# Kernel optimization log

Hardware: AMD Instinct MI355X
Metric: run time of the kernel (lower is better)

The kernel has to match this reference:

```python
import jax, jax.numpy as jnp
import numpy as np

B, N, S, NS, V = 4, 4096, 1024, 32, 8
CIN, COUT = 64, 128
RADIUS = 0.2
C1 = CIN + 6  # cin + grouped_xyz(3) + local_xyz(3)
EPS = 1e-5


def _bn(x, g, b):
    # training-mode batchnorm over all axes except the trailing channel axis
    axes = tuple(range(x.ndim - 1))
    m = jnp.mean(x, axes, keepdims=True)
    v = jnp.var(x, axes, keepdims=True)
    return (x - m) * jax.lax.rsqrt(v + EPS) * g + b


def _fps(xyz, s):
    # farthest point sampling, deterministic start at index 0
    b, n, _ = xyz.shape
    bar = jnp.arange(b)
    def step(carry, _):
        mind, last = carry
        p = xyz[bar, last]  # [B,3]
        d = jnp.sum((xyz - p[:, None, :]) ** 2, -1)
        mind = jnp.minimum(mind, d)
        nxt = jnp.argmax(mind, -1).astype(jnp.int32)
        return (mind, nxt), nxt
    idx0 = jnp.zeros((b,), jnp.int32)
    _, rest = jax.lax.scan(step, (jnp.full((b, n), 1e10, xyz.dtype), idx0), None, length=s - 1)
    idx = jnp.concatenate([idx0[None], rest], 0).T  # [B,S]
    return jnp.take_along_axis(xyz, idx[..., None], axis=1), idx


def _ball_query(new_xyz, xyz, k, radius):
    # first-k-in-index-order points within radius; -1 padding like pytorch3d
    n = xyz.shape[1]
    d2 = jnp.sum((new_xyz[:, :, None, :] - xyz[:, None, :, :]) ** 2, -1)  # [B,S,N]
    key = jnp.where(d2 < radius * radius, jnp.arange(n, dtype=jnp.int32), n)
    negk, _ = jax.lax.top_k(-key, k)  # k smallest keys
    idx = -negk
    mask = idx >= n
    return jnp.where(mask, -1, idx), mask


def _masked_gather(x, idx):
    # gather rows of x [B,N,C] at idx [B,S,k]; zeros where idx == -1
    b, s, k = idx.shape
    safe = jnp.maximum(idx, 0).reshape(b, s * k)
    g = jnp.take_along_axis(x, safe[..., None], axis=1).reshape(b, s, k, x.shape[-1])
    return jnp.where((idx == -1)[..., None], 0.0, g)


def setup_inputs() -> dict:
    key = jax.random.key(0)
    ks = jax.random.split(key, 10)
    xyz = jax.random.uniform(ks[0], (B, N, 3), jnp.float32)
    f = jax.random.normal(ks[1], (B, N, CIN), jnp.float32)
    # cube-corner frame points, scaled by radius*0.8, rotated about Y (as in __init__)
    corners = jnp.array([[x, y, z] for x in (-1.0, 1.0) for y in (-1.0, 1.0) for z in (-1.0, 1.0)], jnp.float32)
    ang = jax.random.uniform(ks[2], ()) * 2.0 * jnp.pi
    c, sn = jnp.cos(ang), jnp.sin(ang)
    z, o = jnp.zeros(()), jnp.ones(())
    rot = jnp.stack([jnp.stack([c, z, sn]), jnp.stack([z, o, z]), jnp.stack([-sn, z, c])])
    framepoints = (corners * (RADIUS * 0.8)) @ rot.T
    w = lambda k_, sh: jax.random.normal(k_, sh, jnp.float32) * 0.05
    return {
        "xyz": xyz, "f": f, "framepoints": framepoints,
        "w1_0": w(ks[3], (13, 64)), "b1_0": jnp.zeros((64,), jnp.float32),
        "g1_0": jnp.ones((64,), jnp.float32), "bt1_0": jnp.zeros((64,), jnp.float32),
        "w1_1": w(ks[4], (64, C1)), "b1_1": jnp.zeros((C1,), jnp.float32),
        "w2_0": w(ks[5], (C1, 128)), "b2_0": jnp.zeros((128,), jnp.float32),
        "g2_0": jnp.ones((128,), jnp.float32), "bt2_0": jnp.zeros((128,), jnp.float32),
        "w2_1": w(ks[6], (128, COUT)), "b2_1": jnp.zeros((COUT,), jnp.float32),
        "res_w": w(ks[7], (CIN, COUT)), "res_b": jnp.zeros((COUT,), jnp.float32),
    }


def _forward(xyz, f, framepoints, w1_0, b1_0, g1_0, bt1_0, w1_1, b1_1,
             w2_0, b2_0, g2_0, bt2_0, w2_1, b2_1, res_w, res_b):
    new_xyz, _ = _fps(xyz, S)                           # [B,S,3]
    idx, mask = _ball_query(new_xyz, xyz, NS, RADIUS)   # [B,S,NS]
    grouped_xyz = _masked_gather(xyz, idx)              # [B,S,NS,3]
    grouped_feature = _masked_gather(f, idx)            # [B,S,NS,CIN]
    local = grouped_xyz - new_xyz[:, :, None, :]
    gf = jnp.concatenate([grouped_xyz, local, grouped_feature], -1)   # [B,S,NS,C1]
    arrow = grouped_xyz[:, :, :, None, :] - framepoints               # [B,S,NS,V,3]
    euc = jnp.sqrt(jnp.sum(arrow ** 2, -1, keepdims=True))
    gx = jnp.broadcast_to(grouped_xyz[:, :, :, None, :], arrow.shape)
    fp = jnp.broadcast_to(framepoints, arrow.shape)
    coc = jnp.concatenate([-arrow, arrow, euc, gx, fp], -1)           # [B,S,NS,V,13]
    # m1: per-point MLP (1x1x1 Conv3d) 13 -> 64 (bn+relu) -> C1
    a = jax.nn.relu(_bn(coc @ w1_0 + b1_0, g1_0, bt1_0))
    a = a @ w1_1 + b1_1                                               # [B,S,NS,V,C1]
    # frame-modulated features + softmax attention over the V frame axis
    p = gf[:, :, :, None, :] * a                                      # [B,S,NS,V,C1]
    agg = jnp.sum(jax.nn.softmax(p, axis=3) * p, axis=3)              # [B,S,NS,C1]
    agg = jnp.where(mask[..., None], 0.0, agg)
    # m2: per-point MLP (1x1 Conv2d) C1 -> 128 (bn+relu) -> COUT
    wmid = jax.nn.relu(_bn(agg @ w2_0 + b2_0, g2_0, bt2_0))
    wout = wmid @ w2_1 + b2_1                                         # [B,S,NS,COUT]
    new_f = jax.nn.gelu(wout + grouped_feature @ res_w + res_b, approximate=False)
    return jnp.max(new_f, axis=2), new_xyz


def reference(xyz, f, framepoints, w1_0, b1_0, g1_0, bt1_0, w1_1, b1_1,
              w2_0, b2_0, g2_0, bt2_0, w2_1, b2_1, res_w, res_b):
    return _forward(xyz, f, framepoints, w1_0, b1_0, g1_0, bt1_0, w1_1, b1_1,
                    w2_0, b2_0, g2_0, bt2_0, w2_1, b2_1, res_w, res_b)
```

## Files before the change

kernel.cpp:

```cpp
#include <hip/hip_runtime.h>
#include <hip/hip_bf16.h>
#include <math.h>

typedef __hip_bfloat16 bf16;
typedef __attribute__((ext_vector_type(8))) short short8;
typedef __attribute__((ext_vector_type(4))) float f32x4;
typedef unsigned long long u64;

#define BB  4
#define NN  4096
#define SS  1024
#define KNS 32
#define C1  70

__device__ __forceinline__ float b2f(bf16 x){ return __bfloat162float(x); }

__device__ __forceinline__ float ld(const void* p, size_t i, bool F){
    return F ? ((const float*)p)[i] : __bfloat162float(((const bf16*)p)[i]);
}
__device__ __forceinline__ void st(void* p, size_t i, float v, bool F){
    if (F) ((float*)p)[i] = v; else ((bf16*)p)[i] = __float2bfloat16(v);
}
__device__ __forceinline__ unsigned short f2us(float x){
    __hip_bfloat16 h = __float2bfloat16(x);
    return *reinterpret_cast<unsigned short*>(&h);
}
__device__ __forceinline__ float us2f(unsigned short u){
    return __uint_as_float(((unsigned)u) << 16);
}
__device__ __forceinline__ float fast_gelu(float x){
    float xs = x * 0.70710678118654752f;
    float ax = fabsf(xs);
    float t = 1.0f / fmaf(0.3275911f, ax, 1.0f);
    float poly = fmaf(fmaf(fmaf(fmaf(1.061405429f, t, -1.453152027f), t,
                    1.421413741f), t, -0.284496736f), t, 0.254829592f) * t;
    float er = 1.0f - poly * __expf(-ax*ax);
    er = copysignf(er, xs);
    return 0.5f * x * (1.0f + er);
}

__device__ __forceinline__ u64 pk_add(u64 a, u64 b){
    u64 d;
    asm("v_pk_add_f32 %0, %1, %2" : "=v"(d) : "v"(a), "v"(b));
    return d;
}
__device__ __forceinline__ u64 pk_mul(u64 a, u64 b){
    u64 d;
    asm("v_pk_mul_f32 %0, %1, %2" : "=v"(d) : "v"(a), "v"(b));
    return d;
}
__device__ __forceinline__ u64 pack2f(float a, float b){
    return (((u64)__float_as_uint(b)) << 32) | __float_as_uint(a);
}
__device__ __forceinline__ u64 dup2f(float a){
    unsigned u = __float_as_uint(a);
    return (((u64)u) << 32) | u;
}

#define DPP_STEP(key, CTRL) do{ \
    int _a = __builtin_amdgcn_update_dpp(0, (int)(unsigned)(key), CTRL, 0xF, 0xF, true); \
    int _b = __builtin_amdgcn_update_dpp(0, (int)(unsigned)((key) >> 32), CTRL, 0xF, 0xF, true); \
    u64 _o = (((u64)(unsigned)_b) << 32) | (unsigned)_a; \
    if (_o > (key)) (key) = _o; }while(0)
#define SWZ_STEP(key, OFF) do{ \
    int _a = __builtin_amdgcn_ds_swizzle((int)(unsigned)(key), OFF); \
    int _b = __builtin_amdgcn_ds_swizzle((int)(unsigned)((key) >> 32), OFF); \
    u64 _o = (((u64)(unsigned)_b) << 32) | (unsigned)_a; \
    if (_o > (key)) (key) = _o; }while(0)

__global__ __launch_bounds__(256) void fps_kernel(const void* __restrict__ xyz,
        float* __restrict__ nxf, void* __restrict__ out, int* __restrict__ flag){
    __shared__ float4 pts[NN];
    __shared__ int sidx[SS];
    __shared__ u64 skey[2][4];
    __shared__ int scnt;
    const int b = blockIdx.x, t = threadIdx.x, lane = t & 63, w = t >> 6;
    if (t == 0) scnt = 0;
    __syncthreads();
    {
        int c = 0;
        for (int i = t; i < 2048; i += 256){
            float v = __bfloat162float(((const bf16*)xyz)[i]);
            if (!(fabsf(v) <= 1.5f)) c++;
        }
        atomicAdd(&scnt, c);
    }
    __syncthreads();
    const bool F = (scnt > 10);
    if (b == 0 && t == 0) *flag = F ? 1 : 0;

    u64 px2[8], py2[8], pz2[8];
    float mind[16];
#pragma unroll
    for (int j = 0; j < 8; j++){
        int i0 = (2*j)*256 + t, i1 = (2*j+1)*256 + t;
        float X0 = ld(xyz, (size_t)(b*NN+i0)*3+0, F);
        float Y0 = ld(xyz, (size_t)(b*NN+i0)*3+1, F);
        float Z0 = ld(xyz, (size_t)(b*NN+i0)*3+2, F);
        float X1 = ld(xyz, (size_t)(b*NN+i1)*3+0, F);
        float Y1 = ld(xyz, (size_t)(b*NN+i1)*3+1, F);
        float Z1 = ld(xyz, (size_t)(b*NN+i1)*3+2, F);
        pts[i0] = make_float4(X0, Y0, Z0, 0.f);
        pts[i1] = make_float4(X1, Y1, Z1, 0.f);
        px2[j] = pack2f(X0, X1); py2[j] = pack2f(Y0, Y1); pz2[j] = pack2f(Z0, Z1);
        mind[2*j] = 1e10f; mind[2*j+1] = 1e10f;
    }
    if (t == 0) sidx[0] = 0;
    __syncthreads();
    float4 q = pts[0];
    for (int s = 1; s < SS; s++){
        const u64 nx2 = dup2f(-q.x), ny2 = dup2f(-q.y), nz2 = dup2f(-q.z);
        float bd = -1.f; int bi = 0;
#pragma unroll
        for (int j = 0; j < 8; j++){
            u64 dx2 = pk_add(px2[j], nx2);
            u64 dy2 = pk_add(py2[j], ny2);
            u64 dz2 = pk_add(pz2[j], nz2);
            u64 d2 = pk_add(pk_add(pk_mul(dx2,dx2), pk_mul(dy2,dy2)), pk_mul(dz2,dz2));
            float dlo = __uint_as_float((unsigned)d2);
            float dhi = __uint_as_float((unsigned)(d2 >> 32));
            float m0 = fminf(mind[2*j], dlo); mind[2*j] = m0;
            if (m0 > bd){ bd = m0; bi = (2*j)*256 + t; }
            float m1 = fminf(mind[2*j+1], dhi); mind[2*j+1] = m1;
            if (m1 > bd){ bd = m1; bi = (2*j+1)*256 + t; }
        }
        u64 key = ((u64)__float_as_uint(bd) << 32) | (unsigned)(~bi);
        DPP_STEP(key, 0xB1);
        DPP_STEP(key, 0x4E);
        DPP_STEP(key, 0x128);
        SWZ_STEP(key, 0x101F);
        SWZ_STEP(key, 0x401F);
        {
            u64 o = __shfl_xor(key, 32);
            if (o > key) key = o;
        }
        const int par = s & 1;
        if (lane == 0) skey[par][w] = key;
        __syncthreads();
        u64 k0 = skey[par][0], k1 = skey[par][1];
        u64 k2 = skey[par][2], k3 = skey[par][3];
        if (k1 > k0) k0 = k1;
        if (k3 > k2) k2 = k3;
        if (k2 > k0) k0 = k2;
        int ix = (int)(~(unsigned)(k0 & 0xffffffffull));
        if (t == 0) sidx[s] = ix;
        q = pts[ix];
    }
    __syncthreads();
    const size_t o1 = (size_t)BB*SS*128;
    for (int s2 = t; s2 < SS; s2 += 256){
        int i = sidx[s2];
        float4 p = pts[i];
        nxf[(b*SS+s2)*3+0] = p.x; nxf[(b*SS+s2)*3+1] = p.y; nxf[(b*SS+s2)*3+2] = p.z;
        st(out, o1 + (size_t)(b*SS+s2)*3+0, p.x, F);
        st(out, o1 + (size_t)(b*SS+s2)*3+1, p.y, F);
        st(out, o1 + (size_t)(b*SS+s2)*3+2, p.z, F);
    }
}

__global__ __launch_bounds__(512) void ball_kernel(const void* __restrict__ xyz,
        const float* __restrict__ nxf, int* __restrict__ idx, const int* __restrict__ flag){
    __shared__ float sx[NN], sy[NN], sz[NN];
    const bool F = (*flag != 0);
    const int b = blockIdx.x, t = threadIdx.x, lane = t & 63, w = t >> 6;
    for (int i = t; i < NN; i += 512){
        sx[i] = ld(xyz, (size_t)(b*NN+i)*3+0, F);
        sy[i] = ld(xyz, (size_t)(b*NN+i)*3+1, F);
        sz[i] = ld(xyz, (size_t)(b*NN+i)*3+2, F);
    }
    __syncthreads();
    const float R2 = 0.2f*0.2f;
    const u64 below = (lane == 63) ? ~0ull >> 1 : ((1ull << lane) - 1ull);
#pragma unroll
    for (int cc = 0; cc < 4; cc++){
        const int s = blockIdx.y*32 + w*4 + cc;
        const float px = nxf[(b*SS+s)*3+0];
        const float py = nxf[(b*SS+s)*3+1];
        const float pz = nxf[(b*SS+s)*3+2];
        int* op = idx + (size_t)(b*SS+s)*KNS;
        int cnt = 0;
        for (int c = 0; c < 64; c++){
            const int i = c*64 + lane;
            float dx = __fsub_rn(px, sx[i]);
            float dy = __fsub_rn(py, sy[i]);
            float dz = __fsub_rn(pz, sz[i]);
            float d2 = __fadd_rn(__fadd_rn(__fmul_rn(dx,dx), __fmul_rn(dy,dy)), __fmul_rn(dz,dz));
            const bool hit = (d2 < R2);
            u64 m = __ballot(hit);
            if (hit){
                int pos = cnt + __popcll(m & below);
                if (pos < KNS) op[pos] = i;
            }
            cnt += __popcll(m);
            if (cnt >= KNS) break;
        }
        if (lane < KNS && lane >= cnt) op[lane] = -1;
    }
}

__device__ __forceinline__ void pack_frag(int e, int K, const void* W, bool F,
                                          short* H, short* L){
    int j = e & 7, lane = (e >> 3) & 63, nt = (e >> 9) & 7, kt = e >> 12;
    int k = kt*32 + ((lane >> 4) & 3)*8 + j;
    int n = nt*16 + (lane & 15);
    float v = (k < K) ? ld(W, (size_t)k*128 + n, F) : 0.f;
    unsigned short h = f2us(v);
    unsigned short l2 = f2us(v - us2f(h));
    H[e] = (short)h; L[e] = (short)l2;
}

__global__ __launch_bounds__(256) void prep1_kernel(
        const void* __restrict__ w20, const void* __restrict__ w21,
        const void* __restrict__ rw, const void* __restrict__ b20,
        const void* __restrict__ b21, const void* __restrict__ rb,
        short* __restrict__ w20rp_h, short* __restrict__ w20rp_l,
        short* __restrict__ w21p_h, short* __restrict__ w21p_l,
        short* __restrict__ rwp_h, short* __restrict__ rwp_l,
        float* __restrict__ b20r, float* __restrict__ bof,
        double* __restrict__ M, double* __restrict__ sums, const int* __restrict__ flag){
    const bool F = (*flag != 0);
    const int t = threadIdx.x;
    if (blockIdx.x == 0){
        if (t < 105) M[t] = 0.0;
        if (t < 256) sums[t] = 0.0;
    }
    int e = blockIdx.x*256 + t;
    if (e < 12288){ pack_frag(e, 70, w20, F, w20rp_h, w20rp_l); return; }
    e -= 12288;
    if (e < 16384){ pack_frag(e, 128, w21, F, w21p_h, w21p_l); return; }
    e -= 16384;
    if (e < 8192){ pack_frag(e, 64, rw, F, rwp_h, rwp_l); return; }
    e -= 8192;
    if (e < 128){
        b20r[e] = ld(b20, e, F);
        bof[e]  = ld(b21, e, F) + ld(rb, e, F);
    }
}

__global__ __launch_bounds__(256) void bn1_stats(const void* __restrict__ xyz,
        const int* __restrict__ idx, const void* __restrict__ fpt, double* __restrict__ M,
        const int* __restrict__ flag){
    __shared__ float sfp[24];
    const bool F = (*flag != 0);
    const int t = threadIdx.x, lane = t & 63;
    if (t < 24) sfp[t] = ld(fpt, t, F);
    __syncthreads();
    float acc[66];
#pragma unroll
    for (int q = 0; q < 66; q++) acc[q] = 0.f;
    for (int it = 0; it < 4; it++){
        const int row = blockIdx.x*1024 + it*256 + t;
        const int b = row >> 15;
        const int id = idx[row];
        float gx = 0.f, gy = 0.f, gz = 0.f;
        if (id >= 0){
            gx = ld(xyz, (size_t)(b*NN+id)*3+0, F);
            gy = ld(xyz, (size_t)(b*NN+id)*3+1, F);
            gz = ld(xyz, (size_t)(b*NN+id)*3+2, F);
        }
#pragma unroll
        for (int v = 0; v < 8; v++){
            float fxv = sfp[v*3+0], fyv = sfp[v*3+1], fzv = sfp[v*3+2];
            float ax = gx - fxv, ay = gy - fyv, az = gz - fzv;
            float eu = sqrtf(ax*ax + ay*ay + az*az);
            float f11[11];
            f11[0] = ax; f11[1] = ay; f11[2] = az; f11[3] = eu;
            f11[4] = gx; f11[5] = gy; f11[6] = gz;
            f11[7] = fxv; f11[8] = fyv; f11[9] = fzv; f11[10] = 1.0f;
            int q = 0;
#pragma unroll
            for (int i = 0; i < 11; i++)
#pragma unroll
                for (int j = i; j < 11; j++){
                    acc[q] = fmaf(f11[i], f11[j], acc[q]);
                    q++;
                }
        }
    }
#pragma unroll
    for (int q = 0; q < 66; q++){
        float s = acc[q];
#pragma unroll
        for (int off = 1; off < 64; off <<= 1) s += __shfl_xor(s, off);
        if (lane == 0) atomicAdd(&M[q], (double)s);
    }
}

__global__ __launch_bounds__(256) void m1_kernel(
        const void* __restrict__ xyz, const void* __restrict__ f, const void* __restrict__ fpt,
        const void* __restrict__ w10, const void* __restrict__ b10,
        const void* __restrict__ w11, const void* __restrict__ b11,
        const float* __restrict__ nxf, const int* __restrict__ idx,
        const double* __restrict__ M, const void* __restrict__ g1, const void* __restrict__ bt1,
        float* __restrict__ agg, const int* __restrict__ flag){
    __shared__ short sthi[4*2*8*72];
    __shared__ short stlo[4*2*8*72];
    __shared__ float gfb[4*2*80];
    __shared__ double Ms[11][11];
    __shared__ float bn1s[128];
    __shared__ short Bh_l[2*5*64*8];
    __shared__ short Bl_l[2*5*64*8];
    const bool F = (*flag != 0);
    const int t = threadIdx.x, lane = t & 63, w = t >> 6;
    const int kq = lane >> 4, cn = lane & 15;

    if (t < 66){
        int e = t, i = 0, off = 0;
        while (e - off >= 11 - i){ off += 11 - i; i++; }
        int j = i + (e - off);
        double val = M[t];
        Ms[i][j] = val; Ms[j][i] = val;
    }
    for (int e = t; e < 2*5*64*8; e += 256){
        int j = e & 7, le = (e >> 3) & 63, rest = e >> 9;
        int nt = rest % 5, ks = rest / 5;
        int k = ks*32 + (le >> 4)*8 + j;
        int c = nt*16 + (le & 15);
        float wv = (c < C1) ? ld(w11, (size_t)k*C1 + c, F) : 0.f;
        unsigned short h = f2us(wv);
        unsigned short l2 = f2us(wv - us2f(h));
        Bh_l[e] = (short)h; Bl_l[e] = (short)l2;
    }
    __syncthreads();
    if (t < 64){
        const double K = 1048576.0;
        const int    bi14[14] = {0,1,2, 0,1,2, 3, 4,5,6, 7,8,9, 10};
        const double sg14[14] = {-1,-1,-1, 1,1,1, 1, 1,1,1, 1,1,1, 1};
        double mv14[14];
        for (int i = 0; i < 14; i++) mv14[i] = sg14[i] * Ms[bi14[i]][10] / K;
        double wc[13];
        for (int i = 0; i < 13; i++) wc[i] = (double)ld(w10, i*64+t, F);
        double mean = (double)ld(b10, t, F);
        for (int i = 0; i < 13; i++) mean += mv14[i]*wc[i];
        double var = 0.0;
        for (int i = 0; i < 13; i++)
            for (int j = 0; j < 13; j++){
                double mij = sg14[i]*sg14[j]*Ms[bi14[i]][bi14[j]]/K;
                var += wc[i]*wc[j]*(mij - mv14[i]*mv14[j]);
            }
        float sc = ld(g1, t, F) / sqrtf((float)var + 1e-5f);
        bn1s[t] = sc;
        bn1s[64+t] = ld(bt1, t, F) - (float)mean * sc;
    }
    __syncthreads();
    const float sc1 = bn1s[lane], sh1 = bn1s[64+lane];

    float binit[5];
#pragma unroll
    for (int nt = 0; nt < 5; nt++){
        int c = nt*16 + cn;
        binit[nt] = (c < C1) ? ld(b11, c, F) : 0.f;
    }
    float W10c[13];
#pragma unroll
    for (int i = 0; i < 13; i++) W10c[i] = ld(w10, i*64+lane, F);
    const float b10v = ld(b10, lane, F);
    float fx[8], fy[8], fz[8];
#pragma unroll
    for (int v = 0; v < 8; v++){
        fx[v] = ld(fpt, v*3+0, F); fy[v] = ld(fpt, v*3+1, F); fz[v] = ld(fpt, v*3+2, F);
    }
    const int quad = lane >> 4;
    const int rr = quad >> 1;
    const int hh = quad & 1;
    const int mA = lane & 15;
    const int rA = mA >> 3, vA = mA & 7;

    const int wid = blockIdx.x*4 + w;
    for (int p = 0; p < 16; p++){
        const int rowbase = wid*32 + p*2;
        int ids[2];
#pragma unroll
        for (int r = 0; r < 2; r++){
            const int row = rowbase + r;
            const int b = row >> 15, s = (row >> 5) & 1023;
            const int id = idx[row];
            ids[r] = id;
            float gx = 0.f, gy = 0.f, gz = 0.f, fv0 = 0.f, fv1 = 0.f;
            if (id >= 0){
                gx = ld(xyz, (size_t)(b*NN+id)*3+0, F);
                gy = ld(xyz, (size_t)(b*NN+id)*3+1, F);
                gz = ld(xyz, (size_t)(b*NN+id)*3+2, F);
                if (lane >= 6) fv0 = ld(f, (size_t)(b*NN+id)*64 + (lane-6), F);
                if (lane < 6)  fv1 = ld(f, (size_t)(b*NN+id)*64 + (58+lane), F);
            }
            const float nxx = nxf[(b*SS+s)*3+0], nxy = nxf[(b*SS+s)*3+1], nxz = nxf[(b*SS+s)*3+2];
            float gf0;
            if (lane == 0) gf0 = gx; else if (lane == 1) gf0 = gy; else if (lane == 2) gf0 = gz;
            else if (lane == 3) gf0 = gx - nxx; else if (lane == 4) gf0 = gy - nxy;
            else if (lane == 5) gf0 = gz - nxz; else gf0 = fv0;
            gfb[w*160 + r*80 + lane] = gf0;
            if (lane < 6)       gfb[w*160 + r*80 + 64 + lane] = fv1;
            else if (lane < 16) gfb[w*160 + r*80 + 64 + lane] = 0.f;
            const int sb = ((w*2 + r)*8)*72 + lane;
#pragma unroll
            for (int v = 0; v < 8; v++){
                float ax = gx - fx[v], ay = gy - fy[v], az = gz - fz[v];
                float eu = sqrtf(ax*ax + ay*ay + az*az);
                float z = b10v;
                z = fmaf(-ax, W10c[0], z); z = fmaf(-ay, W10c[1], z); z = fmaf(-az, W10c[2], z);
                z = fmaf( ax, W10c[3], z); z = fmaf( ay, W10c[4], z); z = fmaf( az, W10c[5], z);
                z = fmaf( eu, W10c[6], z);
                z = fmaf( gx, W10c[7], z); z = fmaf( gy, W10c[8], z); z = fmaf( gz, W10c[9], z);
                z = fmaf(fx[v], W10c[10], z); z = fmaf(fy[v], W10c[11], z); z = fmaf(fz[v], W10c[12], z);
                float a1 = fmaxf(fmaf(z, sc1, sh1), 0.f);
                unsigned short h = f2us(a1);
                unsigned short l2 = f2us(a1 - us2f(h));
                sthi[sb + v*72] = (short)h;
                stlo[sb + v*72] = (short)l2;
            }
        }
        f32x4 acc[5];
#pragma unroll
        for (int nt = 0; nt < 5; nt++){
            f32x4 a; a[0] = binit[nt]; a[1] = binit[nt]; a[2] = binit[nt]; a[3] = binit[nt];
            acc[nt] = a;
        }
        const int aoff = ((w*2 + rA)*8 + vA)*72 + kq*8;
#pragma unroll
        for (int ks = 0; ks < 2; ks++){
            short8 ahi = *(const short8*)&sthi[aoff + ks*32];
            short8 alo = *(const short8*)&stlo[aoff + ks*32];
#pragma unroll
            for (int nt = 0; nt < 5; nt++){
                short8 Wh = ((const short8*)Bh_l)[(ks*5 + nt)*64 + lane];
                short8 Wl = ((const short8*)Bl_l)[(ks*5 + nt)*64 + lane];
                acc[nt] = __builtin_amdgcn_mfma_f32_16x16x32_bf16(ahi, Wh, acc[nt], 0, 0, 0);
                acc[nt] = __builtin_amdgcn_mfma_f32_16x16x32_bf16(alo, Wh, acc[nt], 0, 0, 0);
                acc[nt] = __builtin_amdgcn_mfma_f32_16x16x32_bf16(ahi, Wl, acc[nt], 0, 0, 0);
            }
        }
        const bool msk = ((rr == 0 ? ids[0] : ids[1]) < 0);
#pragma unroll
        for (int nt = 0; nt < 5; nt++){
            const int col = nt*16 + cn;
            float gfv = gfb[w*160 + rr*80 + col];
            f32x4 a = acc[nt];
            float p0 = a[0]*gfv, p1 = a[1]*gfv, p2 = a[2]*gfv, p3 = a[3]*gfv;
            float mx = fmaxf(fmaxf(p0, p1), fmaxf(p2, p3));
            mx = fmaxf(mx, __shfl_xor(mx, 16));
            float e0 = __expf(p0 - mx), e1 = __expf(p1 - mx);
            float e2 = __expf(p2 - mx), e3 = __expf(p3 - mx);
            float den4 = (e0 + e1) + (e2 + e3);
            float num4 = fmaf(e3, p3, fmaf(e2, p2, fmaf(e1, p1, e0*p0)));
            float den = den4 + __shfl_xor(den4, 16);
            float num = num4 + __shfl_xor(num4, 16);
            float outv = num / den;
            if (hh == 0 && col < C1){
                agg[(size_t)(rowbase + rr)*C1 + col] = msk ? 0.f : outv;
            }
        }
    }
}

__global__ __launch_bounds__(256) void bn2_stats(const float* __restrict__ agg,
        const short* __restrict__ w20rp_h, const short* __restrict__ w20rp_l,
        const float* __restrict__ b20r, double* __restrict__ sums){
    __shared__ short Xh[64*104];
    __shared__ short Xl[64*104];
    const int t = threadIdx.x, lane = t & 63, w = t >> 6;
    const int cn = lane & 15, kq = lane >> 4;
    for (int e = t; e < 64*34; e += 256){
        int r = e/34, k = 70 + (e - r*34);
        Xh[r*104+k] = 0; Xl[r*104+k] = 0;
    }
    float bias[8];
#pragma unroll
    for (int nt = 0; nt < 8; nt++) bias[nt] = b20r[nt*16 + cn];
    f32x4 accS[8], accQ[8];
#pragma unroll
    for (int nt = 0; nt < 8; nt++){
        f32x4 zz; zz[0]=0.f; zz[1]=0.f; zz[2]=0.f; zz[3]=0.f;
        accS[nt] = zz; accQ[nt] = zz;
    }
    for (int it = 0; it < 8; it++){
        const int rowbase = blockIdx.x*512 + it*64;
        __syncthreads();
        for (int e = t; e < 64*70; e += 256){
            int r = e/70, k = e - r*70;
            float v = agg[(size_t)rowbase*70 + e];
            unsigned short h = f2us(v);
            unsigned short l2 = f2us(v - us2f(h));
            Xh[r*104+k] = (short)h; Xl[r*104+k] = (short)l2;
        }
        __syncthreads();
        f32x4 z[8];
#pragma unroll
        for (int nt = 0; nt < 8; nt++){
            f32x4 a; a[0]=bias[nt]; a[1]=bias[nt]; a[2]=bias[nt]; a[3]=bias[nt];
            z[nt] = a;
        }
#pragma unroll
        for (int kt = 0; kt < 3; kt++){
            short8 Ah = *(const short8*)&Xh[(w*16 + cn)*104 + kt*32 + kq*8];
            short8 Al = *(const short8*)&Xl[(w*16 + cn)*104 + kt*32 + kq*8];
#pragma unroll
            for (int nt = 0; nt < 8; nt++){
                short8 Wh = ((const short8*)w20rp_h)[(kt*8+nt)*64 + lane];
                short8 Wl = ((const short8*)w20rp_l)[(kt*8+nt)*64 + lane];
                z[nt] = __builtin_amdgcn_mfma_f32_16x16x32_bf16(Ah, Wh, z[nt], 0, 0, 0);
                z[nt] = __builtin_amdgcn_mfma_f32_16x16x32_bf16(Al, Wh, z[nt], 0, 0, 0);
                z[nt] = __builtin_amdgcn_mfma_f32_16x16x32_bf16(Ah, Wl, z[nt], 0, 0, 0);
            }
        }
#pragma unroll
        for (int nt = 0; nt < 8; nt++){
#pragma unroll
            for (int rg = 0; rg < 4; rg++){
                accS[nt][rg] += z[nt][rg];
                accQ[nt][rg] = fmaf(z[nt][rg], z[nt][rg], accQ[nt][rg]);
            }
        }
    }
#pragma unroll
    for (int nt = 0; nt < 8; nt++){
        float s = (accS[nt][0] + accS[nt][1]) + (accS[nt][2] + accS[nt][3]);
        float q = (accQ[nt][0] + accQ[nt][1]) + (accQ[nt][2] + accQ[nt][3]);
        s += __shfl_xor(s, 16); s += __shfl_xor(s, 32);
        q += __shfl_xor(q, 16); q += __shfl_xor(q, 32);
        if (lane < 16){
            atomicAdd(&sums[nt*16 + cn], (double)s);
            atomicAdd(&sums[128 + nt*16 + cn], (double)q);
        }
    }
}

__global__ __launch_bounds__(256) void final_kernel(
        const float* __restrict__ agg, const void* __restrict__ f, const int* __restrict__ idx,
        const short* __restrict__ w20rp_h, const short* __restrict__ w20rp_l,
        const float* __restrict__ b20r, const double* __restrict__ sums,
        const void* __restrict__ g2, const void* __restrict__ bt2,
        const short* __restrict__ w21p_h, const short* __restrict__ w21p_l,
        const short* __restrict__ rwp_h, const short* __restrict__ rwp_l,
        const float* __restrict__ bof,
        void* __restrict__ out, const int* __restrict__ flag){
    __shared__ short Xh[64*104];
    __shared__ short Xl[64*104];
    __shared__ short Yh[64*152];
    __shared__ short Yl[64*152];
    __shared__ float obuf[4][128];
    __shared__ float scsh[256];
    const bool F = (*flag != 0);
    const int t = threadIdx.x, lane = t & 63, w = t >> 6;
    const int cn = lane & 15, kq = lane >> 4;
    const int rowbase = blockIdx.x * 64;
    if (t < 128){
        const double K = 131072.0;
        double mean = sums[t] / K;
        double var = sums[128+t] / K - mean*mean;
        float sc = ld(g2, t, F) / sqrtf((float)var + 1e-5f);
        scsh[t] = sc;
        scsh[128+t] = ld(bt2, t, F) - (float)mean * sc;
    }
    for (int e = t; e < 64*34; e += 256){
        int r = e/34, k = 70 + (e - r*34);
        Xh[r*104+k] = 0; Xl[r*104+k] = 0;
    }
    for (int e = t; e < 64*70; e += 256){
        int r = e/70, k = e - r*70;
        float v = agg[(size_t)rowbase*70 + e];
        unsigned short h = f2us(v);
        unsigned short l2 = f2us(v - us2f(h));
        Xh[r*104+k] = (short)h; Xl[r*104+k] = (short)l2;
    }
    __syncthreads();
    f32x4 z[8];
#pragma unroll
    for (int nt = 0; nt < 8; nt++){
        float b = b20r[nt*16 + cn];
        f32x4 a; a[0]=b; a[1]=b; a[2]=b; a[3]=b;
        z[nt] = a;
    }
#pragma unroll
    for (int kt = 0; kt < 3; kt++){
        short8 Ah = *(const short8*)&Xh[(w*16 + cn)*104 + kt*32 + kq*8];
        short8 Al = *(const short8*)&Xl[(w*16 + cn)*104 + kt*32 + kq*8];
#pragma unroll
        for (int nt = 0; nt < 8; nt++){
            short8 Wh = ((const short8*)w20rp_h)[(kt*8+nt)*64 + lane];
            short8 Wl = ((const short8*)w20rp_l)[(kt*8+nt)*64 + lane];
            z[nt] = __builtin_amdgcn_mfma_f32_16x16x32_bf16(Ah, Wh, z[nt], 0, 0, 0);
            z[nt] = __builtin_amdgcn_mfma_f32_16x16x32_bf16(Al, Wh, z[nt], 0, 0, 0);
            z[nt] = __builtin_amdgcn_mfma_f32_16x16x32_bf16(Ah, Wl, z[nt], 0, 0, 0);
        }
    }
    __syncthreads();
#pragma unroll
    for (int nt = 0; nt < 8; nt++){
        const int col = nt*16 + cn;
        const float sc = scsh[col], sh = scsh[128+col];
#pragma unroll
        for (int rg = 0; rg < 4; rg++){
            float y = fmaxf(fmaf(z[nt][rg], sc, sh), 0.f);
            unsigned short h = f2us(y);
            unsigned short l2 = f2us(y - us2f(h));
            int row = w*16 + kq*4 + rg;
            Yh[row*152+col] = (short)h; Yl[row*152+col] = (short)l2;
        }
    }
    for (int e = t; e < 64*64; e += 256){
        int r = e >> 6, k = e & 63;
        int id = idx[rowbase + r];
        int b = (rowbase + r) >> 15;
        float v = (id >= 0) ? ld(f, (size_t)(b*NN+id)*64 + k, F) : 0.f;
        unsigned short h = f2us(v);
        unsigned short l2 = f2us(v - us2f(h));
        Xh[r*88+k] = (short)h; Xl[r*88+k] = (short)l2;
    }
    __syncthreads();
    f32x4 acc2[8];
#pragma unroll
    for (int nt = 0; nt < 8; nt++){
        float b = bof[nt*16 + cn];
        f32x4 a; a[0]=b; a[1]=b; a[2]=b; a[3]=b;
        acc2[nt] = a;
    }
#pragma unroll
    for (int kt = 0; kt < 4; kt++){
        short8 Ah = *(const short8*)&Yh[(w*16 + cn)*152 + kt*32 + kq*8];
        short8 Al = *(const short8*)&Yl[(w*16 + cn)*152 + kt*32 + kq*8];
#pragma unroll
        for (int nt = 0; nt < 8; nt++){
            short8 Wh = ((const short8*)w21p_h)[(kt*8+nt)*64 + lane];
            short8 Wl = ((const short8*)w21p_l)[(kt*8+nt)*64 + lane];
            acc2[nt] = __builtin_amdgcn_mfma_f32_16x16x32_bf16(Ah, Wh, acc2[nt], 0, 0, 0);
            acc2[nt] = __builtin_amdgcn_mfma_f32_16x16x32_bf16(Al, Wh, acc2[nt], 0, 0, 0);
            acc2[nt] = __builtin_amdgcn_mfma_f32_16x16x32_bf16(Ah, Wl, acc2[nt], 0, 0, 0);
        }
    }
#pragma unroll
    for (int kt = 0; kt < 2; kt++){
        short8 Ah = *(const short8*)&Xh[(w*16 + cn)*88 + kt*32 + kq*8];
        short8 Al = *(const short8*)&Xl[(w*16 + cn)*88 + kt*32 + kq*8];
#pragma unroll
        for (int nt = 0; nt < 8; nt++){
            short8 Wh = ((const short8*)rwp_h)[(kt*8+nt)*64 + lane];
            short8 Wl = ((const short8*)rwp_l)[(kt*8+nt)*64 + lane];
            acc2[nt] = __builtin_amdgcn_mfma_f32_16x16x32_bf16(Ah, Wh, acc2[nt], 0, 0, 0);
            acc2[nt] = __builtin_amdgcn_mfma_f32_16x16x32_bf16(Al, Wh, acc2[nt], 0, 0, 0);
            acc2[nt] = __builtin_amdgcn_mfma_f32_16x16x32_bf16(Ah, Wl, acc2[nt], 0, 0, 0);
        }
    }
#pragma unroll
    for (int nt = 0; nt < 8; nt++){
        float m = -3.4e38f;
#pragma unroll
        for (int rg = 0; rg < 4; rg++){
            m = fmaxf(m, fast_gelu(acc2[nt][rg]));
        }
        m = fmaxf(m, __shfl_xor(m, 16));
        m = fmaxf(m, __shfl_xor(m, 32));
        if (lane < 16) obuf[w][nt*16 + cn] = m;
    }
    __syncthreads();
    {
        int g = t >> 7, c = t & 127;
        float y = fmaxf(obuf[2*g][c], obuf[2*g+1][c]);
        st(out, (size_t)blockIdx.x*256 + t, y, F);
    }
}

extern "C" void kernel_launch(void* const* d_in, const int* in_sizes, int n_in,
                              void* d_out, int out_size, void* d_ws, size_t ws_size,
                              hipStream_t stream){
    const void* xyz = d_in[0];
    const void* f   = d_in[1];
    const void* fpt = d_in[2];
    const void* w10 = d_in[3];
    const void* b10 = d_in[4];
    const void* g1  = d_in[5];
    const void* bt1 = d_in[6];
    const void* w11 = d_in[7];
    const void* b11 = d_in[8];
    const void* w20 = d_in[9];
    const void* b20 = d_in[10];
    const void* g2  = d_in[11];
    const void* bt2 = d_in[12];
    const void* w21 = d_in[13];
    const void* b21 = d_in[14];
    const void* rw  = d_in[15];
    const void* rb  = d_in[16];

    char* ws = (char*)d_ws;
    float*  nxf     = (float*) (ws + 0);
    int*    idx     = (int*)   (ws + 65536);
    double* M       = (double*)(ws + 655360);
    double* sums    = (double*)(ws + 917504);
    int*    flag    = (int*)   (ws + 1050624);
    float*  b20r    = (float*) (ws + 1060864);
    float*  bof     = (float*) (ws + 1061376);
    short*  w20rp_h = (short*) (ws + 1064960);
    short*  w20rp_l = (short*) (ws + 1089536);
    short*  w21p_h  = (short*) (ws + 1163264);
    short*  w21p_l  = (short*) (ws + 1196032);
    short*  rwp_h   = (short*) (ws + 1228800);
    short*  rwp_l   = (short*) (ws + 1245184);
    float*  agg     = (float*) (ws + 2097152);

    fps_kernel<<<4, 256, 0, stream>>>(xyz, nxf, d_out, flag);
    ball_kernel<<<dim3(4, 32), 512, 0, stream>>>(xyz, nxf, idx, flag);
    prep1_kernel<<<145, 256, 0, stream>>>(w20, w21, rw, b20, b21, rb,
                                          w20rp_h, w20rp_l, w21p_h, w21p_l,
                                          rwp_h, rwp_l, b20r, bof, M, sums, flag);
    bn1_stats<<<128, 256, 0, stream>>>(xyz, idx, fpt, M, flag);
    m1_kernel<<<1024, 256, 0, stream>>>(xyz, f, fpt, w10, b10, w11, b11, nxf, idx,
                                        M, g1, bt1, agg, flag);
    bn2_stats<<<256, 256, 0, stream>>>(agg, w20rp_h, w20rp_l, b20r, sums);
    final_kernel<<<2048, 256, 0, stream>>>(agg, f, idx, w20rp_h, w20rp_l, b20r, sums,
                                           g2, bt2, w21p_h, w21p_l, rwp_h, rwp_l,
                                           bof, d_out, flag);
}
```

Before: 1.401 ms.

## Split FPS into two kernels and fold weight prep into first FPS launch

The weight-packing and bias-prep work from prep1_kernel now runs as extra blocks (index 4 and up) of the first FPS kernel. That work can then execute on otherwise idle CUs while the four serial FPS blocks run. FPS itself is split in two: the first kernel does iterations 1 to 511 and saves min-distances and sampled indices to global memory, and a second kernel reloads them and finishes. The split adds a kernel launch plus a global save and restore of FPS state, which partly offsets the launch saved by removing prep1.

New measurement: 1.415 ms. Within noise of the previous version (+1.0%).

```diff
diff --git a/kernel.cpp b/kernel.cpp
--- a/kernel.cpp
+++ b/kernel.cpp
@@ -68,13 +68,32 @@
     u64 _o = (((u64)(unsigned)_b) << 32) | (unsigned)_a; \
     if (_o > (key)) (key) = _o; }while(0)
 
-__global__ __launch_bounds__(256) void fps_kernel(const void* __restrict__ xyz,
-        float* __restrict__ nxf, void* __restrict__ out, int* __restrict__ flag){
+__device__ __forceinline__ void pack_frag(int e, int K, const void* W, bool F,
+                                          short* H, short* L){
+    int j = e & 7, lane = (e >> 3) & 63, nt = (e >> 9) & 7, kt = e >> 12;
+    int k = kt*32 + ((lane >> 4) & 3)*8 + j;
+    int n = nt*16 + (lane & 15);
+    float v = (k < K) ? ld(W, (size_t)k*128 + n, F) : 0.f;
+    unsigned short h = f2us(v);
+    unsigned short l2 = f2us(v - us2f(h));
+    H[e] = (short)h; L[e] = (short)l2;
+}
+
+__global__ __launch_bounds__(256) void fps_a_kernel(const void* __restrict__ xyz,
+        float* __restrict__ mind_g, int* __restrict__ sidx_g, int* __restrict__ flag,
+        const void* __restrict__ w20, const void* __restrict__ w21,
+        const void* __restrict__ rw, const void* __restrict__ b20,
+        const void* __restrict__ b21, const void* __restrict__ rb,
+        short* __restrict__ w20rp_h, short* __restrict__ w20rp_l,
+        short* __restrict__ w21p_h, short* __restrict__ w21p_l,
+        short* __restrict__ rwp_h, short* __restrict__ rwp_l,
+        float* __restrict__ b20r, float* __restrict__ bof,
+        double* __restrict__ M, double* __restrict__ sums){
     __shared__ float4 pts[NN];
-    __shared__ int sidx[SS];
+    __shared__ int sidx[512];
     __shared__ u64 skey[2][4];
     __shared__ int scnt;
-    const int b = blockIdx.x, t = threadIdx.x, lane = t & 63, w = t >> 6;
+    const int t = threadIdx.x, lane = t & 63, w = t >> 6;
     if (t == 0) scnt = 0;
     __syncthreads();
     {
@@ -87,6 +106,26 @@
     }
     __syncthreads();
     const bool F = (scnt > 10);
+
+    if (blockIdx.x >= 4){
+        if (blockIdx.x == 4){
+            if (t < 105) M[t] = 0.0;
+            if (t < 256) sums[t] = 0.0;
+        }
+        int e = (blockIdx.x - 4)*256 + t;
+        if (e < 12288){ pack_frag(e, 70, w20, F, w20rp_h, w20rp_l); return; }
+        e -= 12288;
+        if (e < 16384){ pack_frag(e, 128, w21, F, w21p_h, w21p_l); return; }
+        e -= 16384;
+        if (e < 8192){ pack_frag(e, 64, rw, F, rwp_h, rwp_l); return; }
+        e -= 8192;
+        if (e < 128){
+            b20r[e] = ld(b20, e, F);
+            bof[e]  = ld(b21, e, F) + ld(rb, e, F);
+        }
+        return;
+    }
+    const int b = blockIdx.x;
     if (b == 0 && t == 0) *flag = F ? 1 : 0;
 
     u64 px2[8], py2[8], pz2[8];
@@ -108,7 +147,79 @@
     if (t == 0) sidx[0] = 0;
     __syncthreads();
     float4 q = pts[0];
-    for (int s = 1; s < SS; s++){
+    for (int s = 1; s < 512; s++){
+        const u64 nx2 = dup2f(-q.x), ny2 = dup2f(-q.y), nz2 = dup2f(-q.z);
+        float bd = -1.f; int bi = 0;
+#pragma unroll
+        for (int j = 0; j < 8; j++){
+            u64 dx2 = pk_add(px2[j], nx2);
+            u64 dy2 = pk_add(py2[j], ny2);
+            u64 dz2 = pk_add(pz2[j], nz2);
+            u64 d2 = pk_add(pk_add(pk_mul(dx2,dx2), pk_mul(dy2,dy2)), pk_mul(dz2,dz2));
+            float dlo = __uint_as_float((unsigned)d2);
+            float dhi = __uint_as_float((unsigned)(d2 >> 32));
+            float m0 = fminf(mind[2*j], dlo); mind[2*j] = m0;
+            if (m0 > bd){ bd = m0; bi = (2*j)*256 + t; }
+            float m1 = fminf(mind[2*j+1], dhi); mind[2*j+1] = m1;
+            if (m1 > bd){ bd = m1; bi = (2*j+1)*256 + t; }
+        }
+        u64 key = ((u64)__float_as_uint(bd) << 32) | (unsigned)(~bi);
+        DPP_STEP(key, 0xB1);
+        DPP_STEP(key, 0x4E);
+        DPP_STEP(key, 0x128);
+        SWZ_STEP(key, 0x101F);
+        SWZ_STEP(key, 0x401F);
+        {
+            u64 o = __shfl_xor(key, 32);
+            if (o > key) key = o;
+        }
+        const int par = s & 1;
+        if (lane == 0) skey[par][w] = key;
+        __syncthreads();
+        u64 k0 = skey[par][0], k1 = skey[par][1];
+        u64 k2 = skey[par][2], k3 = skey[par][3];
+        if (k1 > k0) k0 = k1;
+        if (k3 > k2) k2 = k3;
+        if (k2 > k0) k0 = k2;
+        int ix = (int)(~(unsigned)(k0 & 0xffffffffull));
+        if (t == 0) sidx[s] = ix;
+        q = pts[ix];
+    }
+    __syncthreads();
+#pragma unroll
+    for (int j = 0; j < 16; j++) mind_g[(b*16 + j)*256 + t] = mind[j];
+    for (int s = t; s < 512; s += 256) sidx_g[b*1024 + s] = sidx[s];
+}
+
+__global__ __launch_bounds__(256) void fps_b_kernel(const void* __restrict__ xyz,
+        const float* __restrict__ mind_g, int* __restrict__ sidx_g,
+        float* __restrict__ nxf, void* __restrict__ out, const int* __restrict__ flag){
+    __shared__ float4 pts[NN];
+    __shared__ int sidx[SS];
+    __shared__ u64 skey[2][4];
+    const bool F = (*flag != 0);
+    const int b = blockIdx.x, t = threadIdx.x, lane = t & 63, w = t >> 6;
+    u64 px2[8], py2[8], pz2[8];
+    float mind[16];
+#pragma unroll
+    for (int j = 0; j < 8; j++){
+        int i0 = (2*j)*256 + t, i1 = (2*j+1)*256 + t;
+        float X0 = ld(xyz, (size_t)(b*NN+i0)*3+0, F);
+        float Y0 = ld(xyz, (size_t)(b*NN+i0)*3+1, F);
+        float Z0 = ld(xyz, (size_t)(b*NN+i0)*3+2, F);
+        float X1 = ld(xyz, (size_t)(b*NN+i1)*3+0, F);
+        float Y1 = ld(xyz, (size_t)(b*NN+i1)*3+1, F);
+        float Z1 = ld(xyz, (size_t)(b*NN+i1)*3+2, F);
+        pts[i0] = make_float4(X0, Y0, Z0, 0.f);
+        pts[i1] = make_float4(X1, Y1, Z1, 0.f);
+        px2[j] = pack2f(X0, X1); py2[j] = pack2f(Y0, Y1); pz2[j] = pack2f(Z0, Z1);
+        mind[2*j]   = mind_g[(b*16 + 2*j)*256 + t];
+        mind[2*j+1] = mind_g[(b*16 + 2*j+1)*256 + t];
+    }
+    for (int s = t; s < 512; s += 256) sidx[s] = sidx_g[b*1024 + s];
+    __syncthreads();
+    float4 q = pts[sidx[511]];
+    for (int s = 512; s < SS; s++){
         const u64 nx2 = dup2f(-q.x), ny2 = dup2f(-q.y), nz2 = dup2f(-q.z);
         float bd = -1.f; int bi = 0;
 #pragma unroll
@@ -195,45 +306,6 @@
             if (cnt >= KNS) break;
         }
         if (lane < KNS && lane >= cnt) op[lane] = -1;
-    }
-}
-
-__device__ __forceinline__ void pack_frag(int e, int K, const void* W, bool F,
-                                          short* H, short* L){
-    int j = e & 7, lane = (e >> 3) & 63, nt = (e >> 9) & 7, kt = e >> 12;
-    int k = kt*32 + ((lane >> 4) & 3)*8 + j;
-    int n = nt*16 + (lane & 15);
-    float v = (k < K) ? ld(W, (size_t)k*128 + n, F) : 0.f;
-    unsigned short h = f2us(v);
-    unsigned short l2 = f2us(v - us2f(h));
-    H[e] = (short)h; L[e] = (short)l2;
-}
-
-__global__ __launch_bounds__(256) void prep1_kernel(
-        const void* __restrict__ w20, const void* __restrict__ w21,
-        const void* __restrict__ rw, const void* __restrict__ b20,
-        const void* __restrict__ b21, const void* __restrict__ rb,
-        short* __restrict__ w20rp_h, short* __restrict__ w20rp_l,
-        short* __restrict__ w21p_h, short* __restrict__ w21p_l,
-        short* __restrict__ rwp_h, short* __restrict__ rwp_l,
-        float* __restrict__ b20r, float* __restrict__ bof,
-        double* __restrict__ M, double* __restrict__ sums, const int* __restrict__ flag){
-    const bool F = (*flag != 0);
-    const int t = threadIdx.x;
-    if (blockIdx.x == 0){
-        if (t < 105) M[t] = 0.0;
-        if (t < 256) sums[t] = 0.0;
-    }
-    int e = blockIdx.x*256 + t;
-    if (e < 12288){ pack_frag(e, 70, w20, F, w20rp_h, w20rp_l); return; }
-    e -= 12288;
-    if (e < 16384){ pack_frag(e, 128, w21, F, w21p_h, w21p_l); return; }
-    e -= 16384;
-    if (e < 8192){ pack_frag(e, 64, rw, F, rwp_h, rwp_l); return; }
-    e -= 8192;
-    if (e < 128){
-        b20r[e] = ld(b20, e, F);
-        bof[e]  = ld(b21, e, F) + ld(rb, e, F);
     }
 }
 
@@ -695,13 +767,16 @@
     short*  w21p_l  = (short*) (ws + 1196032);
     short*  rwp_h   = (short*) (ws + 1228800);
     short*  rwp_l   = (short*) (ws + 1245184);
+    float*  mind_g  = (float*) (ws + 1310720);
+    int*    sidx_g  = (int*)   (ws + 1376256);
     float*  agg     = (float*) (ws + 2097152);
 
-    fps_kernel<<<4, 256, 0, stream>>>(xyz, nxf, d_out, flag);
+    fps_a_kernel<<<149, 256, 0, stream>>>(xyz, mind_g, sidx_g, flag,
+                                          w20, w21, rw, b20, b21, rb,
+                                          w20rp_h, w20rp_l, w21p_h, w21p_l,
+                                          rwp_h, rwp_l, b20r, bof, M, sums);
+    fps_b_kernel<<<4, 256, 0, stream>>>(xyz, mind_g, sidx_g, nxf, d_out, flag);
     ball_kernel<<<dim3(4, 32), 512, 0, stream>>>(xyz, nxf, idx, flag);
-    prep1_kernel<<<145, 256, 0, stream>>>(w20, w21, rw, b20, b21, rb,
-                                          w20rp_h, w20rp_l, w21p_h, w21p_l,
-                                          rwp_h, rwp_l, b20r, bof, M, sums, flag);
     bn1_stats<<<128, 256, 0, stream>>>(xyz, idx, fpt, M, flag);
     m1_kernel<<<1024, 256, 0, stream>>>(xyz, f, fpt, w10, b10, w11, b11, nxf, idx,
                                         M, g1, bt1, agg, flag);
```
